# Optimization experiments

Measured on AMD Instinct MI355X. Metric: run time of the kernel, lower is better.

The kernel has to match this reference:

```python
import jax, jax.numpy as jnp
import numpy as np

HID, H, KV, S, B = 2048, 32, 8, 2048, 2
D = HID // H           # head_dim = 64
G = H // KV            # query heads per kv head = 4


def setup_inputs() -> dict:
    key = jax.random.key(0)
    ks = jax.random.split(key, 10)
    sc = 0.02
    kv_dim = HID * KV // H  # 512
    return {
        "x": jax.random.normal(ks[0], (B, S, HID), jnp.float32),
        "attention_mask": jnp.zeros((B, S), jnp.float32),
        "Wq": jax.random.normal(ks[1], (HID, HID), jnp.float32) * sc,
        "bq": jnp.zeros((HID,), jnp.float32),
        "Wk": jax.random.normal(ks[2], (kv_dim, HID), jnp.float32) * sc,
        "bk": jnp.zeros((kv_dim,), jnp.float32),
        "Wv": jax.random.normal(ks[3], (kv_dim, HID), jnp.float32) * sc,
        "bv": jnp.zeros((kv_dim,), jnp.float32),
        "Wo": jax.random.normal(ks[4], (HID, HID), jnp.float32) * sc,
        "bo": jnp.zeros((HID,), jnp.float32),
    }


def reference(x, attention_mask, Wq, bq, Wk, bk, Wv, bv, Wo, bo):
    Bx, Sx, _ = x.shape
    # projections (torch Linear: x @ W.T + b)
    q = x @ Wq.T + bq                                  # [B,S,HID]
    k = x @ Wk.T + bk                                  # [B,S,KV*D]
    v = x @ Wv.T + bv
    # split heads: [B,S,H,D] -> [B,H,S,D]; then group q: [B,KV,G,S,D]
    q = q.reshape(Bx, Sx, H, D).transpose(0, 2, 1, 3).reshape(Bx, KV, G, Sx, D)
    k = k.reshape(Bx, Sx, KV, D).transpose(0, 2, 1, 3)  # [B,KV,S,D]
    v = v.reshape(Bx, Sx, KV, D).transpose(0, 2, 1, 3)
    scale = 1.0 / jnp.sqrt(jnp.float32(D))
    scores = jnp.einsum('bkgsd,bktd->bkgst', q, k) * scale  # [B,KV,G,S,S]
    scores = scores + attention_mask[:, None, None, None, :]
    attn = jax.nn.softmax(scores, axis=-1)
    out = jnp.einsum('bkgst,bktd->bkgsd', attn, v)          # [B,KV,G,S,D]
    out = out.reshape(Bx, H, Sx, D).transpose(0, 2, 1, 3).reshape(Bx, Sx, HID)
    return out @ Wo.T + bo
```

## Files before the change

kernel.cpp:

```cpp
#include <hip/hip_runtime.h>
#include <hip/hip_bf16.h>
#include <stdint.h>

typedef __hip_bfloat16 bf16;
typedef __attribute__((ext_vector_type(8))) short bf16x8;
typedef __attribute__((ext_vector_type(4))) float f32x4;
typedef __attribute__((ext_vector_type(16))) float f32x16;
typedef __attribute__((ext_vector_type(4))) int i32x4;
typedef __attribute__((ext_vector_type(2))) int i32x2;

#define B_   2
#define S_   2048
#define HID_ 2048
#define H_   32
#define KV_  8
#define D_   64
#define NT_  (S_ / 64)
#define LOG2E 1.4426950408889634f

__device__ __forceinline__ void gload_lds16(const void* g, void* l) {
  __builtin_amdgcn_global_load_lds(
      (const __attribute__((address_space(1))) uint32_t*)g,
      (__attribute__((address_space(3))) uint32_t*)l, 16, 0, 0);
}
__device__ __forceinline__ float fexp2(float x) { return __builtin_amdgcn_exp2f(x); }

__device__ __forceinline__ uint32_t cvtpk_bf16(float lo, float hi) {
  uint32_t r;
  asm("v_cvt_pk_bf16_f32 %0, %1, %2" : "=v"(r) : "v"(lo), "v"(hi));
  return r;
}
__device__ __forceinline__ void plane32_swap(uint32_t& a, uint32_t& b) {
  i32x2 r = __builtin_amdgcn_permlane32_swap((int)a, (int)b, false, false);
  a = (uint32_t)r[0]; b = (uint32_t)r[1];
}

struct CvtJob { const float* s; bf16* d; int n4; };
__global__ __launch_bounds__(256) void cvt_multi(
    CvtJob j0, CvtJob j1, CvtJob j2, CvtJob j3, CvtJob j4) {
  CvtJob j;
  switch (blockIdx.y) {
    case 0: j = j0; break;
    case 1: j = j1; break;
    case 2: j = j2; break;
    case 3: j = j3; break;
    default: j = j4; break;
  }
  int i = blockIdx.x * blockDim.x + threadIdx.x;
  const int stride = gridDim.x * blockDim.x;
  for (; i < j.n4; i += stride) {
    float4 v = ((const float4*)j.s)[i];
    bf16 t[4];
    t[0] = __float2bfloat16(v.x);
    t[1] = __float2bfloat16(v.y);
    t[2] = __float2bfloat16(v.z);
    t[3] = __float2bfloat16(v.w);
    *reinterpret_cast<uint64_t*>(j.d + 4 * (size_t)i) = *reinterpret_cast<uint64_t*>(t);
  }
}

__global__ __launch_bounds__(256) void mask_prep(
    const float* __restrict__ m, float* __restrict__ o, int n) {
  int i = blockIdx.x * blockDim.x + threadIdx.x;
  if (i < n) o[i] = m[i] * LOG2E;
}

__global__ __launch_bounds__(256, 3) void gemm_qkv(
    const bf16* __restrict__ A,
    const bf16* __restrict__ Wqp, const bf16* __restrict__ Wkp, const bf16* __restrict__ Wvp,
    const float* __restrict__ bqp, const float* __restrict__ bkp, const float* __restrict__ bvp,
    bf16* __restrict__ Cq, bf16* __restrict__ Ck, bf16* __restrict__ Cv) {
  const int lid0 = blockIdx.y * gridDim.x + blockIdx.x;
  const int q8 = (int)(gridDim.x * gridDim.y) >> 3;
  const int lid = (lid0 & 7) * q8 + (lid0 >> 3);
  const int bm = lid & 31;
  const int bn_all = lid >> 5;

  const bf16* W; const float* bias; int bn;
  if (bn_all < 16)      { W = Wqp; bias = bqp; bn = bn_all; }
  else if (bn_all < 20) { W = Wkp; bias = bkp; bn = bn_all - 16; }
  else                  { W = Wvp; bias = bvp; bn = bn_all - 20; }
  const float oscale = (bn_all < 16) ? (0.125f * LOG2E) : 1.0f;

  __shared__ __align__(16) bf16 As[128 * 64];
  __shared__ __align__(16) bf16 Bs[128 * 64];
  const int tid = threadIdx.x;
  const int lane = tid & 63, wid = tid >> 6;
  const int wr = wid >> 1, wc = wid & 1;
  const int K = HID_;

  f32x4 acc[4][4] = {};

  for (int k0 = 0; k0 < K; k0 += 64) {
    __syncthreads();
#pragma unroll
    for (int c = 0; c < 4; ++c) {
      const int r = c * 32 + wid * 8 + (lane >> 3);
      const int gcolb = ((lane & 7) * 16) ^ ((r & 7) << 4);
      gload_lds16(A + (size_t)(bm * 128 + r) * K + k0 + (gcolb >> 1),
                  &As[(c * 32 + wid * 8) * 64]);
      gload_lds16(W + (size_t)(bn * 128 + r) * K + k0 + (gcolb >> 1),
                  &Bs[(c * 32 + wid * 8) * 64]);
    }
    __syncthreads();
#pragma unroll
    for (int ks = 0; ks < 2; ++ks) {
      bf16x8 af[4], bfr[4];
#pragma unroll
      for (int i = 0; i < 4; ++i) {
        const int ra = wr * 64 + i * 16 + (lane & 15);
        const int ka = (ks * 64 + ((lane >> 4) << 4)) ^ ((ra & 7) << 4);
        af[i] = *(const bf16x8*)((const char*)As + ra * 128 + ka);
        const int rb = wc * 64 + i * 16 + (lane & 15);
        const int kb = (ks * 64 + ((lane >> 4) << 4)) ^ ((rb & 7) << 4);
        bfr[i] = *(const bf16x8*)((const char*)Bs + rb * 128 + kb);
      }
      __builtin_amdgcn_s_setprio(1);
#pragma unroll
      for (int i = 0; i < 4; ++i)
#pragma unroll
        for (int j = 0; j < 4; ++j)
          acc[i][j] = __builtin_amdgcn_mfma_f32_16x16x32_bf16(af[i], bfr[j], acc[i][j], 0, 0, 0);
      __builtin_amdgcn_s_setprio(0);
    }
  }

  if (bn_all < 20) {
    const int Hn = (bn_all < 16) ? H_ : KV_;
    bf16* C = (bn_all < 16) ? Cq : Ck;
#pragma unroll
    for (int j = 0; j < 4; ++j) {
      const int n = bn * 128 + wc * 64 + j * 16 + (lane & 15);
      const float bv = bias[n];
#pragma unroll
      for (int i = 0; i < 4; ++i) {
        const int mb = bm * 128 + wr * 64 + i * 16 + ((lane >> 4) << 2);
#pragma unroll
        for (int e = 0; e < 4; ++e) {
          const int m = mb + e;
          const float v = (acc[i][j][e] + bv) * oscale;
          const int b = m >> 11, s = m & (S_ - 1);
          const int h = n >> 6, d = n & 63;
          C[(((size_t)b * Hn + h) * S_ + s) * 64 + d] = __float2bfloat16(v);
        }
      }
    }
  } else {
#pragma unroll
    for (int j = 0; j < 4; ++j) {
      const int n = bn * 128 + wc * 64 + j * 16 + (lane & 15);
      const int kvh = n >> 6, d = n & 63;
      const float bv = bias[n];
#pragma unroll
      for (int i = 0; i < 4; ++i) {
        const int m0 = bm * 128 + wr * 64 + i * 16 + ((lane >> 4) << 2);
        const int b = m0 >> 11, s0 = m0 & (S_ - 1);
        bf16 t4[4];
#pragma unroll
        for (int e = 0; e < 4; ++e) t4[e] = __float2bfloat16(acc[i][j][e] + bv);
        *reinterpret_cast<uint64_t*>(
            Cv + (((size_t)b * KV_ + kvh) * D_ + d) * S_ + s0) =
            *reinterpret_cast<uint64_t*>(t4);
      }
    }
  }
}

__global__ __launch_bounds__(256, 2) void gemm_out(
    const bf16* __restrict__ A, const bf16* __restrict__ W,
    const float* __restrict__ bias, float* __restrict__ C) {
  const int lid0 = blockIdx.y * gridDim.x + blockIdx.x;
  const int q8 = (int)(gridDim.x * gridDim.y) >> 3;
  const int lid = (lid0 & 7) * q8 + (lid0 >> 3);
  const int bm = lid & 31;
  const int bn = lid >> 5;

  __shared__ __align__(16) bf16 As[128 * 64];
  __shared__ __align__(16) bf16 Bs[128 * 64];
  const int tid = threadIdx.x;
  const int lane = tid & 63, wid = tid >> 6;
  const int wr = wid >> 1, wc = wid & 1;
  const int K = HID_, N = HID_;

  f32x4 acc[4][4] = {};

  for (int k0 = 0; k0 < K; k0 += 64) {
    __syncthreads();
#pragma unroll
    for (int c = 0; c < 4; ++c) {
      const int r = c * 32 + wid * 8 + (lane >> 3);
      const int gcolb = ((lane & 7) * 16) ^ ((r & 7) << 4);
      gload_lds16(A + (size_t)(bm * 128 + r) * K + k0 + (gcolb >> 1),
                  &As[(c * 32 + wid * 8) * 64]);
      gload_lds16(W + (size_t)(bn * 128 + r) * K + k0 + (gcolb >> 1),
                  &Bs[(c * 32 + wid * 8) * 64]);
    }
    __syncthreads();
#pragma unroll
    for (int ks = 0; ks < 2; ++ks) {
      bf16x8 af[4], bfr[4];
#pragma unroll
      for (int i = 0; i < 4; ++i) {
        const int ra = wr * 64 + i * 16 + (lane & 15);
        const int ka = (ks * 64 + ((lane >> 4) << 4)) ^ ((ra & 7) << 4);
        af[i] = *(const bf16x8*)((const char*)As + ra * 128 + ka);
        const int rb = wc * 64 + i * 16 + (lane & 15);
        const int kb = (ks * 64 + ((lane >> 4) << 4)) ^ ((rb & 7) << 4);
        bfr[i] = *(const bf16x8*)((const char*)Bs + rb * 128 + kb);
      }
      __builtin_amdgcn_s_setprio(1);
#pragma unroll
      for (int i = 0; i < 4; ++i)
#pragma unroll
        for (int j = 0; j < 4; ++j)
          acc[i][j] = __builtin_amdgcn_mfma_f32_16x16x32_bf16(af[i], bfr[j], acc[i][j], 0, 0, 0);
      __builtin_amdgcn_s_setprio(0);
    }
  }

#pragma unroll
  for (int j = 0; j < 4; ++j) {
    const int n = bn * 128 + wc * 64 + j * 16 + (lane & 15);
    const float bv = bias[n];
#pragma unroll
    for (int i = 0; i < 4; ++i) {
      const int mb = bm * 128 + wr * 64 + i * 16 + ((lane >> 4) << 2);
#pragma unroll
      for (int e = 0; e < 4; ++e) {
        C[(size_t)(mb + e) * N + n] = acc[i][j][e] + bv;
      }
    }
  }
}

__global__ __launch_bounds__(256, 2) void attn_fwd(
    const bf16* __restrict__ qb, const bf16* __restrict__ kb,
    const bf16* __restrict__ vtb, const float* __restrict__ maskL,
    bf16* __restrict__ ob) {
  const int lid0 = blockIdx.y * gridDim.x + blockIdx.x;
  const int q8 = (int)(gridDim.x * gridDim.y) >> 3;
  const int lid = (lid0 & 7) * q8 + (lid0 >> 3);
  const int qtile = lid & 7;
  const int headid = lid >> 3;
  const int b = headid >> 5, h = headid & (H_ - 1);
  const int kv = h >> 2;
  const int tid = threadIdx.x, lane = tid & 63, wid = tid >> 6;
  const int l31 = lane & 31, hi = lane >> 5;

  __shared__ __align__(16) bf16 Ks[2][64 * 64];
  __shared__ __align__(16) bf16 VTs[2][64 * 64];

  const bf16* qh = qb + ((size_t)(b * H_ + h) * S_) * D_;
  const bf16* kh = kb + ((size_t)(b * KV_ + kv) * S_) * D_;
  const bf16* vth = vtb + (size_t)(b * KV_ + kv) * D_ * S_;
  const float* mrow = maskL + (size_t)b * S_;

  const int qrowbase = qtile * 256 + wid * 64;
  bf16x8 qf[2][4];
#pragma unroll
  for (int qs = 0; qs < 2; ++qs)
#pragma unroll
    for (int ks = 0; ks < 4; ++ks)
      qf[qs][ks] = *(const bf16x8*)(qh + (size_t)(qrowbase + qs * 32 + l31) * D_ + ks * 16 + hi * 8);

  bf16x8 ones;
#pragma unroll
  for (int i = 0; i < 8; ++i) ones[i] = (short)0x3F80;

  f32x16 o0[2] = {}, o1[2] = {};
  f32x16 lacc0 = {}, lacc1 = {};

#pragma unroll
  for (int c = 0; c < 2; ++c) {
    const int r = c * 32 + wid * 8 + (lane >> 3);
    const int gcolb = ((lane & 7) * 16) ^ ((r & 7) << 4);
    gload_lds16(kh + (size_t)r * D_ + (gcolb >> 1), &Ks[0][(c * 32 + wid * 8) * 64]);
    gload_lds16(vth + (size_t)r * S_ + (gcolb >> 1), &VTs[0][(c * 32 + wid * 8) * 64]);
  }
  __syncthreads();

  for (int t = 0; t < NT_; ++t) {
    const int cur = t & 1, nxt = cur ^ 1;

    if (t < NT_ - 1) {
#pragma unroll
      for (int c = 0; c < 2; ++c) {
        const int r = c * 32 + wid * 8 + (lane >> 3);
        const int gcolb = ((lane & 7) * 16) ^ ((r & 7) << 4);
        gload_lds16(kh + ((size_t)(t + 1) * 64 + r) * D_ + (gcolb >> 1),
                    &Ks[nxt][(c * 32 + wid * 8) * 64]);
        gload_lds16(vth + (size_t)r * S_ + (t + 1) * 64 + (gcolb >> 1),
                    &VTs[nxt][(c * 32 + wid * 8) * 64]);
      }
    }

    f32x16 s0[2], s1[2];
#pragma unroll
    for (int kbv = 0; kbv < 2; ++kbv) {
#pragma unroll
      for (int rq = 0; rq < 4; ++rq) {
        const f32x4 m4 = *(const f32x4*)(mrow + t * 64 + kbv * 32 + rq * 8 + 4 * hi);
#pragma unroll
        for (int e = 0; e < 4; ++e) {
          s0[kbv][rq * 4 + e] = m4[e];
          s1[kbv][rq * 4 + e] = m4[e];
        }
      }
    }

    bf16x8 kf0[4], kf1[4];
#pragma unroll
    for (int ks = 0; ks < 4; ++ks) {
      const int rk = l31;
      const int kbyte = (ks * 32 + hi * 16) ^ ((rk & 7) << 4);
      kf0[ks] = *(const bf16x8*)((const char*)&Ks[cur][0] + rk * 128 + kbyte);
    }
    __builtin_amdgcn_s_setprio(1);
#pragma unroll
    for (int ks = 0; ks < 4; ++ks)
      s0[0] = __builtin_amdgcn_mfma_f32_32x32x16_bf16(kf0[ks], qf[0][ks], s0[0], 0, 0, 0);
#pragma unroll
    for (int ks = 0; ks < 4; ++ks)
      s1[0] = __builtin_amdgcn_mfma_f32_32x32x16_bf16(kf0[ks], qf[1][ks], s1[0], 0, 0, 0);
    __builtin_amdgcn_s_setprio(0);
#pragma unroll
    for (int ks = 0; ks < 4; ++ks) {
      const int rk = 32 + l31;
      const int kbyte = (ks * 32 + hi * 16) ^ ((rk & 7) << 4);
      kf1[ks] = *(const bf16x8*)((const char*)&Ks[cur][0] + rk * 128 + kbyte);
    }
    __builtin_amdgcn_s_setprio(1);
#pragma unroll
    for (int ks = 0; ks < 4; ++ks)
      s0[1] = __builtin_amdgcn_mfma_f32_32x32x16_bf16(kf1[ks], qf[0][ks], s0[1], 0, 0, 0);
    __builtin_amdgcn_s_setprio(0);

    bf16x8 pa0[2][2], pa1[2][2];
#pragma unroll
    for (int r = 0; r < 16; ++r) s0[0][r] = fexp2(s0[0][r]);
    {
      uint32_t a0 = cvtpk_bf16(s0[0][0], s0[0][1]);
      uint32_t b0 = cvtpk_bf16(s0[0][4], s0[0][5]);
      plane32_swap(a0, b0);
      uint32_t a1 = cvtpk_bf16(s0[0][2], s0[0][3]);
      uint32_t b1 = cvtpk_bf16(s0[0][6], s0[0][7]);
      plane32_swap(a1, b1);
      i32x4 t0; t0[0] = (int)a0; t0[1] = (int)a1; t0[2] = (int)b0; t0[3] = (int)b1;
      pa0[0][0] = __builtin_bit_cast(bf16x8, t0);
      uint32_t a2 = cvtpk_bf16(s0[0][8], s0[0][9]);
      uint32_t b2 = cvtpk_bf16(s0[0][12], s0[0][13]);
      plane32_swap(a2, b2);
      uint32_t a3 = cvtpk_bf16(s0[0][10], s0[0][11]);
      uint32_t b3 = cvtpk_bf16(s0[0][14], s0[0][15]);
      plane32_swap(a3, b3);
      i32x4 t1; t1[0] = (int)a2; t1[1] = (int)a3; t1[2] = (int)b2; t1[3] = (int)b3;
      pa0[0][1] = __builtin_bit_cast(bf16x8, t1);
    }

    __builtin_amdgcn_s_setprio(1);
#pragma unroll
    for (int ks = 0; ks < 4; ++ks)
      s1[1] = __builtin_amdgcn_mfma_f32_32x32x16_bf16(kf1[ks], qf[1][ks], s1[1], 0, 0, 0);
    __builtin_amdgcn_s_setprio(0);

#pragma unroll
    for (int r = 0; r < 16; ++r) s0[1][r] = fexp2(s0[1][r]);
    {
      uint32_t a0 = cvtpk_bf16(s0[1][0], s0[1][1]);
      uint32_t b0 = cvtpk_bf16(s0[1][4], s0[1][5]);
      plane32_swap(a0, b0);
      uint32_t a1 = cvtpk_bf16(s0[1][2], s0[1][3]);
      uint32_t b1 = cvtpk_bf16(s0[1][6], s0[1][7]);
      plane32_swap(a1, b1);
      i32x4 t0; t0[0] = (int)a0; t0[1] = (int)a1; t0[2] = (int)b0; t0[3] = (int)b1;
      pa0[1][0] = __builtin_bit_cast(bf16x8, t0);
      uint32_t a2 = cvtpk_bf16(s0[1][8], s0[1][9]);
      uint32_t b2 = cvtpk_bf16(s0[1][12], s0[1][13]);
      plane32_swap(a2, b2);
      uint32_t a3 = cvtpk_bf16(s0[1][10], s0[1][11]);
      uint32_t b3 = cvtpk_bf16(s0[1][14], s0[1][15]);
      plane32_swap(a3, b3);
      i32x4 t1; t1[0] = (int)a2; t1[1] = (int)a3; t1[2] = (int)b2; t1[3] = (int)b3;
      pa0[1][1] = __builtin_bit_cast(bf16x8, t1);
    }

    bf16x8 vf[2][4];
#pragma unroll
    for (int db = 0; db < 2; ++db)
#pragma unroll
      for (int kk = 0; kk < 4; ++kk) {
        const int kbv = kk >> 1, ks2 = kk & 1;
        const int rd = db * 32 + l31;
        const int vbyte = (kbv * 64 + ks2 * 32 + hi * 16) ^ ((rd & 7) << 4);
        vf[db][kk] = *(const bf16x8*)((const char*)&VTs[cur][0] + rd * 128 + vbyte);
      }

    __builtin_amdgcn_s_setprio(1);
#pragma unroll
    for (int kk = 0; kk < 4; ++kk)
      lacc0 = __builtin_amdgcn_mfma_f32_32x32x16_bf16(pa0[kk >> 1][kk & 1], ones, lacc0, 0, 0, 0);
#pragma unroll
    for (int db = 0; db < 2; ++db)
#pragma unroll
      for (int kk = 0; kk < 4; ++kk)
        o0[db] = __builtin_amdgcn_mfma_f32_32x32x16_bf16(pa0[kk >> 1][kk & 1], vf[db][kk], o0[db], 0, 0, 0);
    __builtin_amdgcn_s_setprio(0);

#pragma unroll
    for (int kbv = 0; kbv < 2; ++kbv) {
#pragma unroll
      for (int r = 0; r < 16; ++r) s1[kbv][r] = fexp2(s1[kbv][r]);
      uint32_t a0 = cvtpk_bf16(s1[kbv][0], s1[kbv][1]);
      uint32_t b0 = cvtpk_bf16(s1[kbv][4], s1[kbv][5]);
      plane32_swap(a0, b0);
      uint32_t a1 = cvtpk_bf16(s1[kbv][2], s1[kbv][3]);
      uint32_t b1 = cvtpk_bf16(s1[kbv][6], s1[kbv][7]);
      plane32_swap(a1, b1);
      i32x4 t0; t0[0] = (int)a0; t0[1] = (int)a1; t0[2] = (int)b0; t0[3] = (int)b1;
      pa1[kbv][0] = __builtin_bit_cast(bf16x8, t0);
      uint32_t a2 = cvtpk_bf16(s1[kbv][8], s1[kbv][9]);
      uint32_t b2 = cvtpk_bf16(s1[kbv][12], s1[kbv][13]);
      plane32_swap(a2, b2);
      uint32_t a3 = cvtpk_bf16(s1[kbv][10], s1[kbv][11]);
      uint32_t b3 = cvtpk_bf16(s1[kbv][14], s1[kbv][15]);
      plane32_swap(a3, b3);
      i32x4 t1; t1[0] = (int)a2; t1[1] = (int)a3; t1[2] = (int)b2; t1[3] = (int)b3;
      pa1[kbv][1] = __builtin_bit_cast(bf16x8, t1);
    }

    __builtin_amdgcn_s_setprio(1);
#pragma unroll
    for (int kk = 0; kk < 4; ++kk)
      lacc1 = __builtin_amdgcn_mfma_f32_32x32x16_bf16(pa1[kk >> 1][kk & 1], ones, lacc1, 0, 0, 0);
#pragma unroll
    for (int db = 0; db < 2; ++db)
#pragma unroll
      for (int kk = 0; kk < 4; ++kk)
        o1[db] = __builtin_amdgcn_mfma_f32_32x32x16_bf16(pa1[kk >> 1][kk & 1], vf[db][kk], o1[db], 0, 0, 0);
    __builtin_amdgcn_s_setprio(0);

    __syncthreads();
  }

#pragma unroll
  for (int r = 0; r < 16; ++r) {
    const int q_out = (r & 3) + 8 * (r >> 2) + 4 * hi;
    {
      const float inv = 1.0f / lacc0[r];
      const int srow = qrowbase + q_out;
      ob[((size_t)b * S_ + srow) * HID_ + h * 64 + l31] = __float2bfloat16(o0[0][r] * inv);
      ob[((size_t)b * S_ + srow) * HID_ + h * 64 + 32 + l31] = __float2bfloat16(o0[1][r] * inv);
    }
    {
      const float inv = 1.0f / lacc1[r];
      const int srow = qrowbase + 32 + q_out;
      ob[((size_t)b * S_ + srow) * HID_ + h * 64 + l31] = __float2bfloat16(o1[0][r] * inv);
      ob[((size_t)b * S_ + srow) * HID_ + h * 64 + 32 + l31] = __float2bfloat16(o1[1][r] * inv);
    }
  }
}

extern "C" void kernel_launch(void* const* d_in, const int* in_sizes, int n_in,
                              void* d_out, int out_size, void* d_ws, size_t ws_size,
                              hipStream_t stream) {
  (void)in_sizes; (void)n_in; (void)out_size; (void)ws_size;
  const float* x  = (const float*)d_in[0];
  const float* am = (const float*)d_in[1];
  const float* Wq = (const float*)d_in[2];
  const float* bq = (const float*)d_in[3];
  const float* Wk = (const float*)d_in[4];
  const float* bk = (const float*)d_in[5];
  const float* Wv = (const float*)d_in[6];
  const float* bv = (const float*)d_in[7];
  const float* Wo = (const float*)d_in[8];
  const float* bo = (const float*)d_in[9];
  float* out = (float*)d_out;

  const size_t XE  = (size_t)B_ * S_ * HID_;
  const size_t WQE = (size_t)HID_ * HID_;
  const size_t WKE = (size_t)(KV_ * D_) * HID_;
  const size_t QE  = (size_t)B_ * H_ * S_ * D_;
  const size_t KE  = (size_t)B_ * KV_ * S_ * D_;

  bf16* xb  = (bf16*)d_ws;
  bf16* wqb = xb + XE;
  bf16* wkb = wqb + WQE;
  bf16* wvb = wkb + WKE;
  bf16* wob = wvb + WKE;
  bf16* qbuf = wob + WQE;
  bf16* kbuf = qbuf + QE;
  bf16* vtbuf = kbuf + KE;
  bf16* abuf = vtbuf + KE;
  float* maskL = (float*)(abuf + XE);

  dim3 blk(256);
  CvtJob jx  = { x,  xb,  (int)(XE / 4) };
  CvtJob jwq = { Wq, wqb, (int)(WQE / 4) };
  CvtJob jwk = { Wk, wkb, (int)(WKE / 4) };
  CvtJob jwv = { Wv, wvb, (int)(WKE / 4) };
  CvtJob jwo = { Wo, wob, (int)(WQE / 4) };
  cvt_multi<<<dim3(512, 5), blk, 0, stream>>>(jx, jwq, jwk, jwv, jwo);
  mask_prep<<<(B_ * S_ + 255) / 256, blk, 0, stream>>>(am, maskL, B_ * S_);

  const int M = B_ * S_;
  gemm_qkv<<<dim3(M / 128, 24), blk, 0, stream>>>(xb, wqb, wkb, wvb, bq, bk, bv,
                                                  qbuf, kbuf, vtbuf);
  attn_fwd<<<dim3(S_ / 256, B_ * H_), blk, 0, stream>>>(qbuf, kbuf, vtbuf, maskL, abuf);
  gemm_out<<<dim3(M / 128, HID_ / 128), blk, 0, stream>>>(abuf, wob, bo, out);
}
```

Baseline: 191.8 us.

## Load K and V tiles directly from global memory, dropping LDS staging and barriers

The attention kernel no longer stages K and V^T tiles through double-buffered shared memory with async global-to-LDS loads. Each wave now reads its MFMA fragments straight from global memory (relying on L1/L2 for reuse across the four waves), which removes the per-iteration __syncthreads. The grid is also flattened to 1D with the same block-index swizzle. The risk is that global latency is exposed without software prefetch, and K/V traffic through the caches rises since every wave reads the full tiles.

```diff
diff --git a/kernel.cpp b/kernel.cpp
--- a/kernel.cpp
+++ b/kernel.cpp
@@ -237,18 +237,15 @@
     const bf16* __restrict__ qb, const bf16* __restrict__ kb,
     const bf16* __restrict__ vtb, const float* __restrict__ maskL,
     bf16* __restrict__ ob) {
-  const int lid0 = blockIdx.y * gridDim.x + blockIdx.x;
-  const int q8 = (int)(gridDim.x * gridDim.y) >> 3;
+  const int tid = threadIdx.x, lane = tid & 63, wid = tid >> 6;
+  const int l31 = lane & 31, hi = lane >> 5;
+  const int lid0 = blockIdx.x;
+  const int q8 = (int)gridDim.x >> 3;
   const int lid = (lid0 & 7) * q8 + (lid0 >> 3);
   const int qtile = lid & 7;
   const int headid = lid >> 3;
   const int b = headid >> 5, h = headid & (H_ - 1);
   const int kv = h >> 2;
-  const int tid = threadIdx.x, lane = tid & 63, wid = tid >> 6;
-  const int l31 = lane & 31, hi = lane >> 5;
-
-  __shared__ __align__(16) bf16 Ks[2][64 * 64];
-  __shared__ __align__(16) bf16 VTs[2][64 * 64];
 
   const bf16* qh = qb + ((size_t)(b * H_ + h) * S_) * D_;
   const bf16* kh = kb + ((size_t)(b * KV_ + kv) * S_) * D_;
@@ -270,29 +267,9 @@
   f32x16 o0[2] = {}, o1[2] = {};
   f32x16 lacc0 = {}, lacc1 = {};
 
-#pragma unroll
-  for (int c = 0; c < 2; ++c) {
-    const int r = c * 32 + wid * 8 + (lane >> 3);
-    const int gcolb = ((lane & 7) * 16) ^ ((r & 7) << 4);
-    gload_lds16(kh + (size_t)r * D_ + (gcolb >> 1), &Ks[0][(c * 32 + wid * 8) * 64]);
-    gload_lds16(vth + (size_t)r * S_ + (gcolb >> 1), &VTs[0][(c * 32 + wid * 8) * 64]);
-  }
-  __syncthreads();
-
   for (int t = 0; t < NT_; ++t) {
-    const int cur = t & 1, nxt = cur ^ 1;
-
-    if (t < NT_ - 1) {
-#pragma unroll
-      for (int c = 0; c < 2; ++c) {
-        const int r = c * 32 + wid * 8 + (lane >> 3);
-        const int gcolb = ((lane & 7) * 16) ^ ((r & 7) << 4);
-        gload_lds16(kh + ((size_t)(t + 1) * 64 + r) * D_ + (gcolb >> 1),
-                    &Ks[nxt][(c * 32 + wid * 8) * 64]);
-        gload_lds16(vth + (size_t)r * S_ + (t + 1) * 64 + (gcolb >> 1),
-                    &VTs[nxt][(c * 32 + wid * 8) * 64]);
-      }
-    }
+    const bf16* kt = kh + (size_t)t * 64 * D_;
+    const bf16* vt = vth + t * 64;
 
     f32x16 s0[2], s1[2];
 #pragma unroll
@@ -308,60 +285,60 @@
       }
     }
 
-    bf16x8 kf0[4], kf1[4];
-#pragma unroll
-    for (int ks = 0; ks < 4; ++ks) {
-      const int rk = l31;
-      const int kbyte = (ks * 32 + hi * 16) ^ ((rk & 7) << 4);
-      kf0[ks] = *(const bf16x8*)((const char*)&Ks[cur][0] + rk * 128 + kbyte);
-    }
-    __builtin_amdgcn_s_setprio(1);
-#pragma unroll
-    for (int ks = 0; ks < 4; ++ks)
-      s0[0] = __builtin_amdgcn_mfma_f32_32x32x16_bf16(kf0[ks], qf[0][ks], s0[0], 0, 0, 0);
-#pragma unroll
-    for (int ks = 0; ks < 4; ++ks)
-      s1[0] = __builtin_amdgcn_mfma_f32_32x32x16_bf16(kf0[ks], qf[1][ks], s1[0], 0, 0, 0);
-    __builtin_amdgcn_s_setprio(0);
-#pragma unroll
-    for (int ks = 0; ks < 4; ++ks) {
-      const int rk = 32 + l31;
-      const int kbyte = (ks * 32 + hi * 16) ^ ((rk & 7) << 4);
-      kf1[ks] = *(const bf16x8*)((const char*)&Ks[cur][0] + rk * 128 + kbyte);
-    }
-    __builtin_amdgcn_s_setprio(1);
-#pragma unroll
-    for (int ks = 0; ks < 4; ++ks)
-      s0[1] = __builtin_amdgcn_mfma_f32_32x32x16_bf16(kf1[ks], qf[0][ks], s0[1], 0, 0, 0);
-    __builtin_amdgcn_s_setprio(0);
+    {
+      bf16x8 kf0[4];
+#pragma unroll
+      for (int ks = 0; ks < 4; ++ks)
+        kf0[ks] = *(const bf16x8*)(kt + (size_t)l31 * D_ + ks * 16 + hi * 8);
+      __builtin_amdgcn_s_setprio(1);
+#pragma unroll
+      for (int ks = 0; ks < 4; ++ks)
+        s0[0] = __builtin_amdgcn_mfma_f32_32x32x16_bf16(kf0[ks], qf[0][ks], s0[0], 0, 0, 0);
+#pragma unroll
+      for (int ks = 0; ks < 4; ++ks)
+        s1[0] = __builtin_amdgcn_mfma_f32_32x32x16_bf16(kf0[ks], qf[1][ks], s1[0], 0, 0, 0);
+      __builtin_amdgcn_s_setprio(0);
+    }
 
     bf16x8 pa0[2][2], pa1[2][2];
-#pragma unroll
-    for (int r = 0; r < 16; ++r) s0[0][r] = fexp2(s0[0][r]);
     {
-      uint32_t a0 = cvtpk_bf16(s0[0][0], s0[0][1]);
-      uint32_t b0 = cvtpk_bf16(s0[0][4], s0[0][5]);
-      plane32_swap(a0, b0);
-      uint32_t a1 = cvtpk_bf16(s0[0][2], s0[0][3]);
-      uint32_t b1 = cvtpk_bf16(s0[0][6], s0[0][7]);
-      plane32_swap(a1, b1);
-      i32x4 t0; t0[0] = (int)a0; t0[1] = (int)a1; t0[2] = (int)b0; t0[3] = (int)b1;
-      pa0[0][0] = __builtin_bit_cast(bf16x8, t0);
-      uint32_t a2 = cvtpk_bf16(s0[0][8], s0[0][9]);
-      uint32_t b2 = cvtpk_bf16(s0[0][12], s0[0][13]);
-      plane32_swap(a2, b2);
-      uint32_t a3 = cvtpk_bf16(s0[0][10], s0[0][11]);
-      uint32_t b3 = cvtpk_bf16(s0[0][14], s0[0][15]);
-      plane32_swap(a3, b3);
-      i32x4 t1; t1[0] = (int)a2; t1[1] = (int)a3; t1[2] = (int)b2; t1[3] = (int)b3;
-      pa0[0][1] = __builtin_bit_cast(bf16x8, t1);
-    }
-
-    __builtin_amdgcn_s_setprio(1);
-#pragma unroll
-    for (int ks = 0; ks < 4; ++ks)
-      s1[1] = __builtin_amdgcn_mfma_f32_32x32x16_bf16(kf1[ks], qf[1][ks], s1[1], 0, 0, 0);
-    __builtin_amdgcn_s_setprio(0);
+      bf16x8 kf1[4];
+#pragma unroll
+      for (int ks = 0; ks < 4; ++ks)
+        kf1[ks] = *(const bf16x8*)(kt + (size_t)(32 + l31) * D_ + ks * 16 + hi * 8);
+      __builtin_amdgcn_s_setprio(1);
+#pragma unroll
+      for (int ks = 0; ks < 4; ++ks)
+        s0[1] = __builtin_amdgcn_mfma_f32_32x32x16_bf16(kf1[ks], qf[0][ks], s0[1], 0, 0, 0);
+      __builtin_amdgcn_s_setprio(0);
+
+#pragma unroll
+      for (int r = 0; r < 16; ++r) s0[0][r] = fexp2(s0[0][r]);
+      {
+        uint32_t a0 = cvtpk_bf16(s0[0][0], s0[0][1]);
+        uint32_t b0 = cvtpk_bf16(s0[0][4], s0[0][5]);
+        plane32_swap(a0, b0);
+        uint32_t a1 = cvtpk_bf16(s0[0][2], s0[0][3]);
+        uint32_t b1 = cvtpk_bf16(s0[0][6], s0[0][7]);
+        plane32_swap(a1, b1);
+        i32x4 t0; t0[0] = (int)a0; t0[1] = (int)a1; t0[2] = (int)b0; t0[3] = (int)b1;
+        pa0[0][0] = __builtin_bit_cast(bf16x8, t0);
+        uint32_t a2 = cvtpk_bf16(s0[0][8], s0[0][9]);
+        uint32_t b2 = cvtpk_bf16(s0[0][12], s0[0][13]);
+        plane32_swap(a2, b2);
+        uint32_t a3 = cvtpk_bf16(s0[0][10], s0[0][11]);
+        uint32_t b3 = cvtpk_bf16(s0[0][14], s0[0][15]);
+        plane32_swap(a3, b3);
+        i32x4 t1; t1[0] = (int)a2; t1[1] = (int)a3; t1[2] = (int)b2; t1[3] = (int)b3;
+        pa0[0][1] = __builtin_bit_cast(bf16x8, t1);
+      }
+
+      __builtin_amdgcn_s_setprio(1);
+#pragma unroll
+      for (int ks = 0; ks < 4; ++ks)
+        s1[1] = __builtin_amdgcn_mfma_f32_32x32x16_bf16(kf1[ks], qf[1][ks], s1[1], 0, 0, 0);
+      __builtin_amdgcn_s_setprio(0);
+    }
 
 #pragma unroll
     for (int r = 0; r < 16; ++r) s0[1][r] = fexp2(s0[1][r]);
@@ -388,12 +365,9 @@
 #pragma unroll
     for (int db = 0; db < 2; ++db)
 #pragma unroll
-      for (int kk = 0; kk < 4; ++kk) {
-        const int kbv = kk >> 1, ks2 = kk & 1;
-        const int rd = db * 32 + l31;
-        const int vbyte = (kbv * 64 + ks2 * 32 + hi * 16) ^ ((rd & 7) << 4);
-        vf[db][kk] = *(const bf16x8*)((const char*)&VTs[cur][0] + rd * 128 + vbyte);
-      }
+      for (int kk = 0; kk < 4; ++kk)
+        vf[db][kk] = *(const bf16x8*)(vt + (size_t)(db * 32 + l31) * S_ +
+                                      (kk >> 1) * 32 + (kk & 1) * 16 + hi * 8);
 
     __builtin_amdgcn_s_setprio(1);
 #pragma unroll
@@ -438,8 +412,6 @@
       for (int kk = 0; kk < 4; ++kk)
         o1[db] = __builtin_amdgcn_mfma_f32_32x32x16_bf16(pa1[kk >> 1][kk & 1], vf[db][kk], o1[db], 0, 0, 0);
     __builtin_amdgcn_s_setprio(0);
-
-    __syncthreads();
   }
 
 #pragma unroll
@@ -505,6 +477,6 @@
   const int M = B_ * S_;
   gemm_qkv<<<dim3(M / 128, 24), blk, 0, stream>>>(xb, wqb, wkb, wvb, bq, bk, bv,
                                                   qbuf, kbuf, vtbuf);
-  attn_fwd<<<dim3(S_ / 256, B_ * H_), blk, 0, stream>>>(qbuf, kbuf, vtbuf, maskL, abuf);
+  attn_fwd<<<dim3((S_ / 256) * B_ * H_), blk, 0, stream>>>(qbuf, kbuf, vtbuf, maskL, abuf);
   gemm_out<<<dim3(M / 128, HID_ / 128), blk, 0, stream>>>(abuf, wob, bo, out);
 }
```

New measurement: 244.5 us. +27.5%, slower.
